# Performance work log

Hardware: AMD Instinct MI355X
Metric: run time of the kernel (lower is better)

The kernel has to match this reference:

```python
import jax, jax.numpy as jnp
import numpy as np

STRIDE = 4
IMG_H, IMG_W = 800, 1216
NMS_THRESH = 0.7
PRE_NMS = 1000
POST_NMS = 1000
MIN_SIZE = 0.0
SCALE_CLAMP = float(np.log(1000.0 / 16.0))  # detectron2 Box2BoxTransform clamp
A = 3  # anchors per location


def _cell_anchors():
    size = 32.0
    ars = jnp.array([0.5, 1.0, 2.0], jnp.float32)
    area = size * size
    w = jnp.sqrt(area / ars)
    h = ars * w
    return jnp.stack([-w / 2, -h / 2, w / 2, h / 2], axis=1)  # [A,4]


def _anchors(H, W):
    sx = jnp.arange(W, dtype=jnp.float32) * STRIDE
    sy = jnp.arange(H, dtype=jnp.float32) * STRIDE
    gy, gx = jnp.meshgrid(sy, sx, indexing='ij')
    shifts = jnp.stack([gx, gy, gx, gy], axis=-1).reshape(-1, 1, 4)  # [H*W,1,4]
    return (shifts + _cell_anchors()[None]).reshape(-1, 4)  # [H*W*A,4]


def _conv(x, w, b, pad):
    y = jax.lax.conv_general_dilated(x, w, (1, 1), pad,
                                     dimension_numbers=('NCHW', 'OIHW', 'NCHW'))
    return y + b[None, :, None, None]


def _decode(anchors, deltas):
    # anchors [M,4], deltas [N,M,4]; weights (1,1,1,1)
    wa = anchors[:, 2] - anchors[:, 0]
    ha = anchors[:, 3] - anchors[:, 1]
    cx = anchors[:, 0] + 0.5 * wa
    cy = anchors[:, 1] + 0.5 * ha
    dx, dy = deltas[..., 0], deltas[..., 1]
    dw = jnp.minimum(deltas[..., 2], SCALE_CLAMP)
    dh = jnp.minimum(deltas[..., 3], SCALE_CLAMP)
    px = dx * wa + cx
    py = dy * ha + cy
    pw = jnp.exp(dw) * wa
    ph = jnp.exp(dh) * ha
    return jnp.stack([px - 0.5 * pw, py - 0.5 * ph,
                      px + 0.5 * pw, py + 0.5 * ph], axis=-1)


def _iou_matrix(boxes):  # [K,4] -> [K,K]
    area = (boxes[:, 2] - boxes[:, 0]) * (boxes[:, 3] - boxes[:, 1])
    lt = jnp.maximum(boxes[:, None, :2], boxes[None, :, :2])
    rb = jnp.minimum(boxes[:, None, 2:], boxes[None, :, 2:])
    wh = jnp.clip(rb - lt, 0.0)
    inter = wh[..., 0] * wh[..., 1]
    return inter / jnp.maximum(area[:, None] + area[None, :] - inter, 1e-9)


def _nms_keep(boxes):
    # boxes already sorted by descending score; greedy NMS
    iou = _iou_matrix(boxes)
    K = boxes.shape[0]

    def step(sup, i):
        keep = ~sup[i]
        sup = sup | (keep & (iou[i] > NMS_THRESH))
        return sup, keep

    _, keep = jax.lax.scan(step, jnp.zeros(K, bool), jnp.arange(K))
    return keep


def setup_inputs() -> dict:
    key = jax.random.key(0)
    ks = jax.random.split(key, 4)
    features = jax.random.normal(ks[0], (2, 256, 200, 304), jnp.float32)
    w_conv = jax.random.normal(ks[1], (256, 256, 3, 3), jnp.float32) * 0.01
    b_conv = jnp.zeros((256,), jnp.float32)
    w_obj = jax.random.normal(ks[2], (3, 256, 1, 1), jnp.float32) * 0.01
    b_obj = jnp.zeros((3,), jnp.float32)
    w_delta = jax.random.normal(ks[3], (12, 256, 1, 1), jnp.float32) * 0.01
    b_delta = jnp.zeros((12,), jnp.float32)
    return {"features": features, "w_conv": w_conv, "b_conv": b_conv,
            "w_obj": w_obj, "b_obj": b_obj, "w_delta": w_delta, "b_delta": b_delta}


def reference(features, w_conv, b_conv, w_obj, b_obj, w_delta, b_delta):
    N, C, H, W = features.shape
    t = jax.nn.relu(_conv(features, w_conv, b_conv, 'SAME'))
    logits = _conv(t, w_obj, b_obj, 'VALID')            # [N,A,H,W]
    deltas = _conv(t, w_delta, b_delta, 'VALID')        # [N,4A,H,W]
    logits = logits.transpose(0, 2, 3, 1).reshape(N, -1)               # [N,H*W*A]
    deltas = deltas.reshape(N, A, 4, H, W).transpose(0, 3, 4, 1, 2).reshape(N, -1, 4)

    anchors = _anchors(H, W)                             # [H*W*A,4]
    boxes = _decode(anchors, deltas)                     # [N,M,4]
    boxes = jnp.stack([jnp.clip(boxes[..., 0], 0.0, IMG_W),
                       jnp.clip(boxes[..., 1], 0.0, IMG_H),
                       jnp.clip(boxes[..., 2], 0.0, IMG_W),
                       jnp.clip(boxes[..., 3], 0.0, IMG_H)], axis=-1)

    valid = ((boxes[..., 2] - boxes[..., 0]) >= MIN_SIZE) & \
            ((boxes[..., 3] - boxes[..., 1]) >= MIN_SIZE)
    scores = jnp.where(valid, logits, -jnp.inf)

    top_s, top_i = jax.lax.top_k(scores, PRE_NMS)                      # sorted desc
    top_b = jnp.take_along_axis(boxes, top_i[..., None], axis=1)       # [N,K,4]

    keep = jax.vmap(_nms_keep)(top_b)                                  # [N,K]
    s = jnp.where(keep, top_s, -jnp.inf)
    fin_s, fin_i = jax.lax.top_k(s, POST_NMS)                          # sorted desc (=final sort)
    fin_b = jnp.take_along_axis(top_b, fin_i[..., None], axis=1)
    fin_b = jnp.where(jnp.isfinite(fin_s)[..., None], fin_b, 0.0)
    return fin_b, fin_s
```

## Files before the change

kernel.cpp:

```cpp
#include <hip/hip_runtime.h>
#include <math.h>
#include <stdint.h>

#define CC 256
#define HH 200
#define WW 304
#define NN 2
#define HW 60800
#define MM 182400
#define KK 1000
#define HP 202
#define WP 306
#define SCALE_CLAMP_F 4.135166556742356f
#define NEG_SENTINEL -1.0e30f
#define CAND_CAP 2048

typedef __attribute__((ext_vector_type(8))) short short8;
typedef __attribute__((ext_vector_type(4))) float f32x4;

#define VMW(N) asm volatile("s_waitcnt vmcnt(" #N ")" ::: "memory")

__device__ __forceinline__ unsigned short f2bf(float f) {
  unsigned u = __float_as_uint(f);
  u += 0x7FFFu + ((u >> 16) & 1u);
  return (unsigned short)(u >> 16);
}
__device__ __forceinline__ unsigned int fkey(float s) {
  unsigned int u = __float_as_uint(s);
  return (u & 0x80000000u) ? ~u : (u | 0x80000000u);
}
__device__ __forceinline__ float iou_ref(float4 a, float4 b) {
#pragma clang fp contract(off)
  float areaA = (a.z - a.x) * (a.w - a.y);
  float areaB = (b.z - b.x) * (b.w - b.y);
  float ltx = fmaxf(a.x, b.x), lty = fmaxf(a.y, b.y);
  float rbx = fminf(a.z, b.z), rby = fminf(a.w, b.w);
  float w = fmaxf(rbx - ltx, 0.0f), h = fmaxf(rby - lty, 0.0f);
  float inter = w * h;
  float denom = fmaxf(areaA + areaB - inter, 1e-9f);
  return inter / denom;
}
__device__ __forceinline__ void gload16(const void* g, void* l) {
  __builtin_amdgcn_global_load_lds(
      (const __attribute__((address_space(1))) unsigned int*)g,
      (__attribute__((address_space(3))) unsigned int*)l, 16, 0, 0);
}
__device__ __forceinline__ int swz(int byte) {
  return byte ^ (((byte >> 7) & 7) << 4);
}

__global__ __launch_bounds__(256) void wt_pack(const float* __restrict__ w,
                                               unsigned short* __restrict__ wt_b) {
  int o = blockIdx.x * 256 + threadIdx.x;
  int cin = o & 255, cout = (o >> 8) & 255, pos = o >> 16;
  wt_b[o] = f2bf(w[(cout * 256 + cin) * 9 + pos]);
}

__global__ __launch_bounds__(256) void in_pack(const float* __restrict__ in,
                                               unsigned short* __restrict__ fbp) {
  __shared__ unsigned short tile[64][65];
  int tid = threadIdx.x;
  int p0 = blockIdx.x * 64;
  int c0 = blockIdx.y * 64;
  int n = blockIdx.z;
  int lane = tid & 63;
  int p = p0 + lane;
  int yp = 0, xp = 0;
  bool inb = false;
  if (p < HP * WP) {
    yp = p / WP; xp = p - yp * WP;
    inb = (yp >= 1 && yp <= HH && xp >= 1 && xp <= WW);
  }
  for (int ci = tid >> 6; ci < 64; ci += 4) {
    float v = 0.f;
    if (inb) v = in[(((size_t)n * CC + c0 + ci) * HH + (yp - 1)) * WW + (xp - 1)];
    tile[ci][lane] = f2bf(v);
  }
  __syncthreads();
  for (int i = 0; i < 4; ++i) {
    int idx4 = (i * 256 + tid) * 4;
    int hwi = idx4 >> 6, cb = idx4 & 63;
    int pp = p0 + hwi;
    if (pp < HP * WP) {
      ushort4 v;
      v.x = tile[cb][hwi]; v.y = tile[cb + 1][hwi];
      v.z = tile[cb + 2][hwi]; v.w = tile[cb + 3][hwi];
      *(ushort4*)&fbp[((size_t)n * HP * WP + pp) * 256 + c0 + cb] = v;
    }
  }
}

__global__ __launch_bounds__(256) void conv_mfma(
    const unsigned short* __restrict__ wt_b, const unsigned short* __restrict__ fbp,
    const float* __restrict__ bias, const float* __restrict__ w_obj,
    const float* __restrict__ w_delta, float* __restrict__ phead) {
  __shared__ __align__(16) unsigned short lA[3][4096];
  __shared__ __align__(16) unsigned short lB[2][5760];
  __shared__ float bl_l[128];
  int tid = threadIdx.x;
  int lane = tid & 63, wid = tid >> 6;
  int wm = wid >> 1, wn = wid & 1;
  int lrow = lane & 15, lgrp = lane >> 4;
  int zz = blockIdx.z;
  int n = zz >> 1, ct = zz & 1;
  int X0 = blockIdx.x * 16, Y0 = blockIdx.y * 8;

  f32x4 acc[4][4];
#pragma unroll
  for (int m = 0; m < 4; ++m)
#pragma unroll
    for (int r = 0; r < 4; ++r) acc[m][r] = {0.f, 0.f, 0.f, 0.f};

  if (tid < 128) bl_l[tid] = bias[ct * 128 + tid];

  auto stageA = [&](int pos, int cc, int buf) {
#pragma unroll
    for (int is = 0; is < 2; ++is) {
      int idx = is * 256 + tid;
      int L = swz(idx * 16);
      int cout = L >> 6, q = (L >> 4) & 3;
      const unsigned short* g =
          wt_b + (((size_t)pos * 256 + ct * 128 + cout) << 8) + cc * 32 + q * 8;
      gload16(g, (char*)&lA[buf][0] + is * 4096 + (wid << 10));
    }
  };
  auto stageB = [&](int cc, int buf) {
#pragma unroll
    for (int is = 0; is < 3; ++is) {
      int idx = is * 256 + tid;
      if (idx < 720) {
        int L = swz(idx * 16);
        int rc = L >> 6, q = (L >> 4) & 3;
        int row = rc / 18, col = rc - row * 18;
        const unsigned short* g =
            fbp + (((size_t)n * HP + Y0 + row) * WP + X0 + col) * 256 + cc * 32 + q * 8;
        gload16(g, (char*)&lB[buf][0] + is * 4096 + (wid << 10));
      }
    }
  };

  stageA(0, 0, 0);
  stageA(1, 0, 1);
  stageB(0, 0);
  __syncthreads();

#pragma unroll 1
  for (int cc = 0; cc < 8; ++cc) {
    const int bb = cc & 1;
    const bool ccl7 = (cc < 7);
#pragma unroll
    for (int pos = 0; pos < 9; ++pos) {
      {
        int pos2 = pos + 2, cc2 = cc;
        if (pos2 >= 9) { pos2 -= 9; cc2 += 1; }
        if (cc2 < 8) stageA(pos2, cc2, (pos + 2) % 3);
      }
      if (pos == 0 && ccl7) stageB(cc + 1, bb ^ 1);

      int ky = pos / 3, kx = pos - ky * 3;
      short8 af[4], bfr[4];
#pragma unroll
      for (int m = 0; m < 4; ++m) {
        int Lb = ((wm * 64 + m * 16 + lrow) << 6) + (lgrp << 4);
        af[m] = *(const short8*)((const char*)&lA[pos % 3][0] + swz(Lb));
      }
#pragma unroll
      for (int r = 0; r < 4; ++r) {
        int Lb = (((wn * 4 + r + ky) * 18 + lrow + kx) << 6) + (lgrp << 4);
        bfr[r] = *(const short8*)((const char*)&lB[bb][0] + swz(Lb));
      }
#pragma unroll
      for (int m = 0; m < 4; ++m)
#pragma unroll
        for (int r = 0; r < 4; ++r)
          acc[m][r] = __builtin_amdgcn_mfma_f32_16x16x32_bf16(af[m], bfr[r], acc[m][r], 0, 0, 0);

      if (pos < 2) {
        if (ccl7) VMW(5); else VMW(2);
      } else if (pos == 7) {
        if (ccl7) VMW(2); else VMW(0);
      } else {
        VMW(2);
      }
      __builtin_amdgcn_sched_barrier(0);
      __builtin_amdgcn_s_barrier();
      asm volatile("" ::: "memory");
    }
  }
  __syncthreads();

#pragma unroll
  for (int m = 0; m < 4; ++m)
#pragma unroll
    for (int j = 0; j < 4; ++j) {
      float b = bl_l[wm * 64 + m * 16 + (lgrp << 2) + j];
#pragma unroll
      for (int r = 0; r < 4; ++r) acc[m][r][j] = fmaxf(acc[m][r][j] + b, 0.f);
    }

  float* whl_l = (float*)&lA[0][0];
  for (int i = tid; i < 1920; i += 256) {
    int o = i >> 7, cl = i & 127;
    whl_l[i] = (o < 3) ? w_obj[o * 256 + ct * 128 + cl]
                       : w_delta[(o - 3) * 256 + ct * 128 + cl];
  }
  __syncthreads();

  float* hacc = (float*)&lB[0][0];
#pragma unroll 1
  for (int o = 0; o < 15; ++o) {
    float p0 = 0.f, p1 = 0.f, p2 = 0.f, p3 = 0.f;
#pragma unroll
    for (int m = 0; m < 4; ++m)
#pragma unroll
      for (int j = 0; j < 4; ++j) {
        float w = whl_l[o * 128 + wm * 64 + m * 16 + (lgrp << 2) + j];
        p0 = fmaf(w, acc[m][0][j], p0);
        p1 = fmaf(w, acc[m][1][j], p1);
        p2 = fmaf(w, acc[m][2][j], p2);
        p3 = fmaf(w, acc[m][3][j], p3);
      }
    p0 += __shfl_xor(p0, 16); p0 += __shfl_xor(p0, 32);
    p1 += __shfl_xor(p1, 16); p1 += __shfl_xor(p1, 32);
    p2 += __shfl_xor(p2, 16); p2 += __shfl_xor(p2, 32);
    p3 += __shfl_xor(p3, 16); p3 += __shfl_xor(p3, 32);
    if (lgrp == 0) {
      hacc[(((o * 8) + wn * 4 + 0) * 16 + lrow) * 2 + wm] = p0;
      hacc[(((o * 8) + wn * 4 + 1) * 16 + lrow) * 2 + wm] = p1;
      hacc[(((o * 8) + wn * 4 + 2) * 16 + lrow) * 2 + wm] = p2;
      hacc[(((o * 8) + wn * 4 + 3) * 16 + lrow) * 2 + wm] = p3;
    }
  }
  __syncthreads();

  if (tid < 128) {
    int row = tid >> 4, col = tid & 15;
    int loc = (Y0 + row) * WW + (X0 + col);
    size_t base = ((size_t)zz * 15) * HW + loc;
#pragma unroll
    for (int o = 0; o < 15; ++o) {
      const float* hp = &hacc[((o * 8 + row) * 16 + col) * 2];
      phead[base + (size_t)o * HW] = hp[0] + hp[1];
    }
  }
}

__global__ __launch_bounds__(256) void decode_kernel(
    const float* __restrict__ phead, const float* __restrict__ b_obj,
    const float* __restrict__ b_delta, float* __restrict__ scores,
    float* __restrict__ boxes, unsigned long long* __restrict__ keys,
    unsigned int* __restrict__ ghist) {
  __shared__ unsigned int hl[8192];
  int tid = threadIdx.x;
  for (int i = tid; i < 8192; i += 256) hl[i] = 0;
  __syncthreads();
  int n = blockIdx.y;
  int loc = blockIdx.x * 256 + tid;
  if (loc < HW) {
    float ho[15];
    const float* p0 = phead + ((size_t)(n * 2 + 0) * 15) * HW + loc;
    const float* p1 = phead + ((size_t)(n * 2 + 1) * 15) * HW + loc;
#pragma unroll
    for (int o = 0; o < 15; ++o) ho[o] = p0[(size_t)o * HW] + p1[(size_t)o * HW];
#pragma unroll
    for (int o = 0; o < 3; ++o) ho[o] += b_obj[o];
#pragma unroll
    for (int o = 0; o < 12; ++o) ho[3 + o] += b_delta[o];
    {
#pragma clang fp contract(off)
      int h = loc / WW, w = loc - h * WW;
      float gx = (float)(w * 4);
      float gy = (float)(h * 4);
      float s2048 = sqrtf(2048.0f), s512 = sqrtf(512.0f);
      float aw[3] = {s2048, 32.0f, s512};
      float ah[3] = {0.5f * s2048, 32.0f, 2.0f * s512};
#pragma unroll
      for (int a = 0; a < 3; ++a) {
        float ax1 = gx - 0.5f * aw[a], ay1 = gy - 0.5f * ah[a];
        float ax2 = gx + 0.5f * aw[a], ay2 = gy + 0.5f * ah[a];
        float wa = ax2 - ax1, ha = ay2 - ay1;
        float cx = ax1 + 0.5f * wa, cy = ay1 + 0.5f * ha;
        float dx = ho[3 + a * 4 + 0], dy = ho[3 + a * 4 + 1];
        float dw = fminf(ho[3 + a * 4 + 2], SCALE_CLAMP_F);
        float dh = fminf(ho[3 + a * 4 + 3], SCALE_CLAMP_F);
        float px = dx * wa + cx, py = dy * ha + cy;
        float pw = expf(dw) * wa, ph = expf(dh) * ha;
        float x1 = px - 0.5f * pw, y1 = py - 0.5f * ph;
        float x2v = px + 0.5f * pw, y2v = py + 0.5f * ph;
        x1 = fminf(fmaxf(x1, 0.f), 1216.f);
        y1 = fminf(fmaxf(y1, 0.f), 800.f);
        x2v = fminf(fmaxf(x2v, 0.f), 1216.f);
        y2v = fminf(fmaxf(y2v, 0.f), 800.f);
        int m = loc * 3 + a;
        ((float4*)boxes)[(size_t)n * MM + m] = make_float4(x1, y1, x2v, y2v);
        float sc = ho[a];
        scores[(size_t)n * MM + m] = sc;
        unsigned long long k =
            ((unsigned long long)fkey(sc) << 18) | (unsigned long long)(262143 - m);
        keys[(size_t)n * MM + m] = k;
        atomicAdd(&hl[(unsigned)(k >> 37)], 1u);
      }
    }
  }
  __syncthreads();
  for (int i = tid; i < 8192; i += 256) {
    unsigned v = hl[i];
    if (v) atomicAdd(&ghist[n * 8192 + i], v);
  }
}

__global__ __launch_bounds__(256) void gather_kernel(
    const unsigned long long* __restrict__ keys, const unsigned int* __restrict__ ghist,
    unsigned int* __restrict__ cnt, unsigned long long* __restrict__ cand) {
  __shared__ unsigned int ps[256];
  __shared__ int bsh;
  int n = blockIdx.y, tid = threadIdx.x;
  const unsigned int* h = ghist + n * 8192;
  unsigned s = 0;
  for (int k = 0; k < 32; ++k) s += h[tid * 32 + k];
  ps[tid] = s;
  __syncthreads();
  if (tid == 0) {
    unsigned cum = 0; int b = 0;
    for (int t = 255; t >= 0; --t) {
      if (cum + ps[t] >= KK) {
        for (int bin = t * 32 + 31; bin >= t * 32; --bin) {
          cum += h[bin];
          if (cum >= KK) { b = bin; break; }
        }
        break;
      }
      cum += ps[t];
    }
    bsh = b;
  }
  __syncthreads();
  int b = bsh;
  const unsigned long long* kp = keys + (size_t)n * MM;
  int i0 = blockIdx.x * 2850, i1 = min(i0 + 2850, MM);
  for (int i = i0 + tid; i < i1; i += 256) {
    unsigned long long k = kp[i];
    if ((int)(unsigned)(k >> 37) >= b) {
      unsigned pos = atomicAdd(&cnt[n], 1u);
      if (pos < CAND_CAP) cand[(size_t)n * CAND_CAP + pos] = k;
    }
  }
}

__global__ __launch_bounds__(1024) void final_select(
    const unsigned long long* __restrict__ cand, const unsigned int* __restrict__ cnt,
    const float* __restrict__ scores, const float* __restrict__ boxes,
    float* __restrict__ s_scores, float* __restrict__ s_boxes) {
  __shared__ unsigned long long sel[CAND_CAP];
  int n = blockIdx.x, tid = threadIdx.x;
  int E = (int)min(cnt[n], (unsigned)CAND_CAP);
  for (int i = tid; i < CAND_CAP; i += 1024)
    sel[i] = (i < E) ? cand[(size_t)n * CAND_CAP + i] : 0ull;
  __syncthreads();
  for (unsigned k2 = 2; k2 <= CAND_CAP; k2 <<= 1) {
    for (unsigned j = k2 >> 1; j > 0; j >>= 1) {
      for (int i = tid; i < CAND_CAP; i += 1024) {
        int l = i ^ (int)j;
        if (l > i) {
          unsigned long long a = sel[i], bb = sel[l];
          bool sw = ((i & k2) == 0) ? (a < bb) : (a > bb);
          if (sw) { sel[i] = bb; sel[l] = a; }
        }
      }
      __syncthreads();
    }
  }
  if (tid < KK) {
    unsigned long long k = sel[tid];
    int m = 262143 - (int)(k & 0x3FFFFull);
    s_scores[n * KK + tid] = scores[(size_t)n * MM + m];
    ((float4*)s_boxes)[n * KK + tid] = ((const float4*)boxes)[(size_t)n * MM + m];
  }
}

__global__ __launch_bounds__(256) void mask_kernel(const float* __restrict__ s_boxes,
                                                   unsigned long long* __restrict__ mask) {
  int i = blockIdx.x, n = blockIdx.y;
  int tid = threadIdx.x, w = tid >> 6, lane = tid & 63;
  const float4* bp = (const float4*)s_boxes + n * KK;
  float4 bi = bp[i];
#pragma unroll
  for (int p = 0; p < 4; ++p) {
    int word = p * 4 + w;
    int j = word * 64 + lane;
    bool over = false;
    if (j < KK) {
      float4 bj = bp[j];
      over = iou_ref(bi, bj) > 0.7f;
    }
    unsigned long long bal = __ballot(over);
    if (lane == 0) mask[((size_t)n * KK + i) * 16 + word] = bal;
  }
}

__global__ __launch_bounds__(1024) void scan_write_kernel(
    const float* __restrict__ s_scores, const float* __restrict__ s_boxes,
    const unsigned long long* __restrict__ mask, float* __restrict__ out) {
  int n = blockIdx.x, tid = threadIdx.x;
  int wid = tid >> 6, lane = tid & 63;
  __shared__ unsigned long long swl[16];
  __shared__ unsigned long long keepw[16];
  __shared__ unsigned int wpre[17];
  if (tid < 16) swl[tid] = 0ull;
  __syncthreads();
  const unsigned long long* mrow = mask + (size_t)n * 16000;
  for (int c = 0; c < 16; ++c) {
    int i = c * 64 + lane;
    unsigned long long myword = (i < KK) ? mrow[(size_t)i * 16 + wid] : 0ull;
    if (wid == 0) {
      unsigned long long m = (i < KK) ? mrow[(size_t)i * 16 + c] : 0ull;
      unsigned long long cur = swl[c];
      unsigned long long kw = 0ull;
      int lim = min(64, KK - c * 64);
      for (int b = 0; b < lim; ++b) {
        unsigned long long mb = __shfl(m, b);
        if (!((cur >> b) & 1ull)) { kw |= (1ull << b); cur |= mb; }
      }
      if (lane == 0) keepw[c] = kw;
    }
    __syncthreads();
    unsigned long long kw = keepw[c];
    unsigned long long v = ((kw >> lane) & 1ull) ? myword : 0ull;
#pragma unroll
    for (int s = 32; s > 0; s >>= 1) v |= __shfl_xor(v, s);
    if (lane == 0) swl[wid] |= v;
    __syncthreads();
  }
  if (tid == 0) {
    unsigned int c = 0;
    for (int w2 = 0; w2 < 16; ++w2) { wpre[w2] = c; c += (unsigned int)__popcll(keepw[w2]); }
    wpre[16] = c;
  }
  __syncthreads();
  if (tid < KK) {
    int word = tid >> 6, bit = tid & 63;
    unsigned long long kwv = keepw[word];
    bool kept = (kwv >> bit) & 1ull;
    unsigned int before = wpre[word] + (unsigned int)__popcll(kwv & ((1ull << bit) - 1ull));
    unsigned int nk = wpre[16];
    unsigned int dst = kept ? before : nk + ((unsigned int)tid - before);
    float4 b = kept ? ((const float4*)s_boxes)[n * KK + tid] : make_float4(0.f, 0.f, 0.f, 0.f);
    float s = kept ? s_scores[n * KK + tid] : NEG_SENTINEL;
    ((float4*)out)[n * KK + dst] = b;
    out[8000 + n * KK + dst] = s;
  }
}

extern "C" void kernel_launch(void* const* d_in, const int* in_sizes, int n_in,
                              void* d_out, int out_size, void* d_ws, size_t ws_size,
                              hipStream_t stream) {
  (void)in_sizes; (void)n_in; (void)out_size; (void)ws_size;
  const float* features = (const float*)d_in[0];
  const float* w_conv   = (const float*)d_in[1];
  const float* b_conv   = (const float*)d_in[2];
  const float* w_obj    = (const float*)d_in[3];
  const float* b_obj    = (const float*)d_in[4];
  const float* w_delta  = (const float*)d_in[5];
  const float* b_delta  = (const float*)d_in[6];

  char* ws = (char*)d_ws;
  unsigned short* wt_b = (unsigned short*)ws;
  unsigned short* fbp  = (unsigned short*)(ws + 1179648);
  char* O = ws + 64475136;
  float* phead = (float*)O;
  float* scores = (float*)(O + 14592000);
  float* boxes  = (float*)(O + 16051200);
  unsigned long long* keys = (unsigned long long*)(O + 21888000);
  char* P = O + 24806400;
  unsigned int* ghist = (unsigned int*)P;
  unsigned int* cnt = (unsigned int*)(P + 65536);
  unsigned long long* cand = (unsigned long long*)(P + 65792);
  float* s_scores = (float*)(P + 98560);
  float* s_boxes  = (float*)(P + 106752);
  unsigned long long* maskbuf = (unsigned long long*)(P + 139264);
  float* out = (float*)d_out;

  wt_pack<<<2304, 256, 0, stream>>>(w_conv, wt_b);
  in_pack<<<dim3(966, 4, 2), 256, 0, stream>>>(features, fbp);
  hipMemsetAsync(ghist, 0, 65536 + 256, stream);
  conv_mfma<<<dim3(19, 25, 4), 256, 0, stream>>>(wt_b, fbp, b_conv, w_obj, w_delta, phead);
  decode_kernel<<<dim3(238, 2), 256, 0, stream>>>(phead, b_obj, b_delta,
                                                  scores, boxes, keys, ghist);
  gather_kernel<<<dim3(64, 2), 256, 0, stream>>>(keys, ghist, cnt, cand);
  final_select<<<2, 1024, 0, stream>>>(cand, cnt, scores, boxes, s_scores, s_boxes);
  mask_kernel<<<dim3(1000, 2), 256, 0, stream>>>(s_boxes, maskbuf);
  scan_write_kernel<<<2, 1024, 0, stream>>>(s_scores, s_boxes, maskbuf, out);
}
```

Measured before the change: 395.6 us.

## Merge pack kernels, simplify conv pipeline, and fuse NMS mask into scan

Three changes land together. The weight pack, input pack and histogram memset become one launch. The conv inner loop drops from a three-stage A buffer with hand-tuned vmcnt waits to two-stage double buffering with plain __syncthreads. The separate IoU mask kernel is removed, and the NMS scan computes IoUs on the fly from boxes held in LDS. This cuts launch overhead and the global mask round trip, but the conv loop loses some latency hiding and the NMS now runs on only two blocks.

```diff
diff --git a/kernel.cpp b/kernel.cpp
--- a/kernel.cpp
+++ b/kernel.cpp
@@ -18,8 +18,6 @@
 typedef __attribute__((ext_vector_type(8))) short short8;
 typedef __attribute__((ext_vector_type(4))) float f32x4;
 
-#define VMW(N) asm volatile("s_waitcnt vmcnt(" #N ")" ::: "memory")
-
 __device__ __forceinline__ unsigned short f2bf(float f) {
   unsigned u = __float_as_uint(f);
   u += 0x7FFFu + ((u >> 16) & 1u);
@@ -49,44 +47,51 @@
   return byte ^ (((byte >> 7) & 7) << 4);
 }
 
-__global__ __launch_bounds__(256) void wt_pack(const float* __restrict__ w,
-                                               unsigned short* __restrict__ wt_b) {
-  int o = blockIdx.x * 256 + threadIdx.x;
-  int cin = o & 255, cout = (o >> 8) & 255, pos = o >> 16;
-  wt_b[o] = f2bf(w[(cout * 256 + cin) * 9 + pos]);
-}
-
-__global__ __launch_bounds__(256) void in_pack(const float* __restrict__ in,
-                                               unsigned short* __restrict__ fbp) {
+__global__ __launch_bounds__(256) void pack_kernel(
+    const float* __restrict__ w, unsigned short* __restrict__ wt_b,
+    const float* __restrict__ in, unsigned short* __restrict__ fbp,
+    unsigned int* __restrict__ ghist, unsigned int* __restrict__ cnt) {
   __shared__ unsigned short tile[64][65];
+  int b = blockIdx.x;
   int tid = threadIdx.x;
-  int p0 = blockIdx.x * 64;
-  int c0 = blockIdx.y * 64;
-  int n = blockIdx.z;
-  int lane = tid & 63;
-  int p = p0 + lane;
-  int yp = 0, xp = 0;
-  bool inb = false;
-  if (p < HP * WP) {
-    yp = p / WP; xp = p - yp * WP;
-    inb = (yp >= 1 && yp <= HH && xp >= 1 && xp <= WW);
-  }
-  for (int ci = tid >> 6; ci < 64; ci += 4) {
-    float v = 0.f;
-    if (inb) v = in[(((size_t)n * CC + c0 + ci) * HH + (yp - 1)) * WW + (xp - 1)];
-    tile[ci][lane] = f2bf(v);
-  }
-  __syncthreads();
-  for (int i = 0; i < 4; ++i) {
-    int idx4 = (i * 256 + tid) * 4;
-    int hwi = idx4 >> 6, cb = idx4 & 63;
-    int pp = p0 + hwi;
-    if (pp < HP * WP) {
-      ushort4 v;
-      v.x = tile[cb][hwi]; v.y = tile[cb + 1][hwi];
-      v.z = tile[cb + 2][hwi]; v.w = tile[cb + 3][hwi];
-      *(ushort4*)&fbp[((size_t)n * HP * WP + pp) * 256 + c0 + cb] = v;
-    }
+  if (b < 2304) {
+    int o = b * 256 + tid;
+    int cin = o & 255, cout = (o >> 8) & 255, pos = o >> 16;
+    wt_b[o] = f2bf(w[(cout * 256 + cin) * 9 + pos]);
+  } else if (b < 10032) {
+    int bb = b - 2304;
+    int bx = bb % 966, rem = bb / 966;
+    int by = rem & 3, n = rem >> 2;
+    int p0 = bx * 64, c0 = by * 64;
+    int lane = tid & 63;
+    int p = p0 + lane;
+    int yp = 0, xp = 0;
+    bool inb = false;
+    if (p < HP * WP) {
+      yp = p / WP; xp = p - yp * WP;
+      inb = (yp >= 1 && yp <= HH && xp >= 1 && xp <= WW);
+    }
+    for (int ci = tid >> 6; ci < 64; ci += 4) {
+      float v = 0.f;
+      if (inb) v = in[(((size_t)n * CC + c0 + ci) * HH + (yp - 1)) * WW + (xp - 1)];
+      tile[ci][lane] = f2bf(v);
+    }
+    __syncthreads();
+    for (int i = 0; i < 4; ++i) {
+      int idx4 = (i * 256 + tid) * 4;
+      int hwi = idx4 >> 6, cb = idx4 & 63;
+      int pp = p0 + hwi;
+      if (pp < HP * WP) {
+        ushort4 v;
+        v.x = tile[cb][hwi]; v.y = tile[cb + 1][hwi];
+        v.z = tile[cb + 2][hwi]; v.w = tile[cb + 3][hwi];
+        *(ushort4*)&fbp[((size_t)n * HP * WP + pp) * 256 + c0 + cb] = v;
+      }
+    }
+  } else {
+    int i = (b - 10032) * 256 + tid;
+    ghist[i] = 0;
+    if (i < 2) cnt[i] = 0;
   }
 }
 
@@ -94,7 +99,7 @@
     const unsigned short* __restrict__ wt_b, const unsigned short* __restrict__ fbp,
     const float* __restrict__ bias, const float* __restrict__ w_obj,
     const float* __restrict__ w_delta, float* __restrict__ phead) {
-  __shared__ __align__(16) unsigned short lA[3][4096];
+  __shared__ __align__(16) unsigned short lA[2][4096];
   __shared__ __align__(16) unsigned short lB[2][5760];
   __shared__ float bl_l[128];
   int tid = threadIdx.x;
@@ -140,29 +145,24 @@
   };
 
   stageA(0, 0, 0);
-  stageA(1, 0, 1);
   stageB(0, 0);
   __syncthreads();
 
+  int ab = 0;
 #pragma unroll 1
   for (int cc = 0; cc < 8; ++cc) {
-    const int bb = cc & 1;
-    const bool ccl7 = (cc < 7);
+    int bb = cc & 1;
 #pragma unroll
     for (int pos = 0; pos < 9; ++pos) {
-      {
-        int pos2 = pos + 2, cc2 = cc;
-        if (pos2 >= 9) { pos2 -= 9; cc2 += 1; }
-        if (cc2 < 8) stageA(pos2, cc2, (pos + 2) % 3);
-      }
-      if (pos == 0 && ccl7) stageB(cc + 1, bb ^ 1);
-
+      if (pos < 8) stageA(pos + 1, cc, ab ^ 1);
+      else if (cc < 7) stageA(0, cc + 1, ab ^ 1);
+      if (pos == 0 && cc < 7) stageB(cc + 1, bb ^ 1);
       int ky = pos / 3, kx = pos - ky * 3;
       short8 af[4], bfr[4];
 #pragma unroll
       for (int m = 0; m < 4; ++m) {
         int Lb = ((wm * 64 + m * 16 + lrow) << 6) + (lgrp << 4);
-        af[m] = *(const short8*)((const char*)&lA[pos % 3][0] + swz(Lb));
+        af[m] = *(const short8*)((const char*)&lA[ab][0] + swz(Lb));
       }
 #pragma unroll
       for (int r = 0; r < 4; ++r) {
@@ -174,20 +174,10 @@
 #pragma unroll
         for (int r = 0; r < 4; ++r)
           acc[m][r] = __builtin_amdgcn_mfma_f32_16x16x32_bf16(af[m], bfr[r], acc[m][r], 0, 0, 0);
-
-      if (pos < 2) {
-        if (ccl7) VMW(5); else VMW(2);
-      } else if (pos == 7) {
-        if (ccl7) VMW(2); else VMW(0);
-      } else {
-        VMW(2);
-      }
-      __builtin_amdgcn_sched_barrier(0);
-      __builtin_amdgcn_s_barrier();
-      asm volatile("" ::: "memory");
-    }
-  }
-  __syncthreads();
+      __syncthreads();
+      ab ^= 1;
+    }
+  }
 
 #pragma unroll
   for (int m = 0; m < 4; ++m)
@@ -378,57 +368,49 @@
   }
 }
 
-__global__ __launch_bounds__(256) void mask_kernel(const float* __restrict__ s_boxes,
-                                                   unsigned long long* __restrict__ mask) {
-  int i = blockIdx.x, n = blockIdx.y;
-  int tid = threadIdx.x, w = tid >> 6, lane = tid & 63;
-  const float4* bp = (const float4*)s_boxes + n * KK;
-  float4 bi = bp[i];
-#pragma unroll
-  for (int p = 0; p < 4; ++p) {
-    int word = p * 4 + w;
-    int j = word * 64 + lane;
-    bool over = false;
-    if (j < KK) {
-      float4 bj = bp[j];
-      over = iou_ref(bi, bj) > 0.7f;
-    }
-    unsigned long long bal = __ballot(over);
-    if (lane == 0) mask[((size_t)n * KK + i) * 16 + word] = bal;
-  }
-}
-
-__global__ __launch_bounds__(1024) void scan_write_kernel(
+__global__ __launch_bounds__(1024) void nms_kernel(
     const float* __restrict__ s_scores, const float* __restrict__ s_boxes,
-    const unsigned long long* __restrict__ mask, float* __restrict__ out) {
+    float* __restrict__ out) {
   int n = blockIdx.x, tid = threadIdx.x;
   int wid = tid >> 6, lane = tid & 63;
+  __shared__ float4 bx[KK];
   __shared__ unsigned long long swl[16];
   __shared__ unsigned long long keepw[16];
   __shared__ unsigned int wpre[17];
+  for (int i = tid; i < KK; i += 1024) bx[i] = ((const float4*)s_boxes)[n * KK + i];
   if (tid < 16) swl[tid] = 0ull;
   __syncthreads();
-  const unsigned long long* mrow = mask + (size_t)n * 16000;
   for (int c = 0; c < 16; ++c) {
-    int i = c * 64 + lane;
-    unsigned long long myword = (i < KK) ? mrow[(size_t)i * 16 + wid] : 0ull;
+    int lim = min(64, KK - c * 64);
     if (wid == 0) {
-      unsigned long long m = (i < KK) ? mrow[(size_t)i * 16 + c] : 0ull;
-      unsigned long long cur = swl[c];
-      unsigned long long kw = 0ull;
-      int lim = min(64, KK - c * 64);
-      for (int b = 0; b < lim; ++b) {
-        unsigned long long mb = __shfl(m, b);
-        if (!((cur >> b) & 1ull)) { kw |= (1ull << b); cur |= mb; }
+      int r = c * 64 + lane;
+      bool rv = r < KK;
+      float4 bi = rv ? bx[r] : make_float4(0.f, 0.f, 0.f, 0.f);
+      unsigned long long wrd = 0ull;
+      for (int j = 0; j < lim; ++j)
+        if (rv && iou_ref(bi, bx[c * 64 + j]) > 0.7f) wrd |= (1ull << j);
+      unsigned long long cur = swl[c], kw = 0ull;
+      for (int bbit = 0; bbit < lim; ++bbit) {
+        unsigned long long mb = __shfl(wrd, bbit);
+        if (!((cur >> bbit) & 1ull)) { kw |= (1ull << bbit); cur |= mb; }
       }
       if (lane == 0) keepw[c] = kw;
     }
     __syncthreads();
     unsigned long long kw = keepw[c];
-    unsigned long long v = ((kw >> lane) & 1ull) ? myword : 0ull;
-#pragma unroll
-    for (int s = 32; s > 0; s >>= 1) v |= __shfl_xor(v, s);
-    if (lane == 0) swl[wid] |= v;
+    int j = wid * 64 + lane;
+    bool jv = j < KK;
+    float4 bj = jv ? bx[j] : make_float4(0.f, 0.f, 0.f, 0.f);
+    bool sup = false;
+    unsigned long long t = kw;
+    while (t) {
+      int bbit = __ffsll((unsigned long long)t) - 1;
+      t &= t - 1;
+      float4 br = bx[c * 64 + bbit];
+      if (iou_ref(br, bj) > 0.7f) sup = true;
+    }
+    unsigned long long bal = __ballot(sup && jv);
+    if (lane == 0) swl[wid] |= bal;
     __syncthreads();
   }
   if (tid == 0) {
@@ -444,7 +426,7 @@
     unsigned int before = wpre[word] + (unsigned int)__popcll(kwv & ((1ull << bit) - 1ull));
     unsigned int nk = wpre[16];
     unsigned int dst = kept ? before : nk + ((unsigned int)tid - before);
-    float4 b = kept ? ((const float4*)s_boxes)[n * KK + tid] : make_float4(0.f, 0.f, 0.f, 0.f);
+    float4 b = kept ? bx[tid] : make_float4(0.f, 0.f, 0.f, 0.f);
     float s = kept ? s_scores[n * KK + tid] : NEG_SENTINEL;
     ((float4*)out)[n * KK + dst] = b;
     out[8000 + n * KK + dst] = s;
@@ -477,17 +459,13 @@
   unsigned long long* cand = (unsigned long long*)(P + 65792);
   float* s_scores = (float*)(P + 98560);
   float* s_boxes  = (float*)(P + 106752);
-  unsigned long long* maskbuf = (unsigned long long*)(P + 139264);
   float* out = (float*)d_out;
 
-  wt_pack<<<2304, 256, 0, stream>>>(w_conv, wt_b);
-  in_pack<<<dim3(966, 4, 2), 256, 0, stream>>>(features, fbp);
-  hipMemsetAsync(ghist, 0, 65536 + 256, stream);
+  pack_kernel<<<10096, 256, 0, stream>>>(w_conv, wt_b, features, fbp, ghist, cnt);
   conv_mfma<<<dim3(19, 25, 4), 256, 0, stream>>>(wt_b, fbp, b_conv, w_obj, w_delta, phead);
   decode_kernel<<<dim3(238, 2), 256, 0, stream>>>(phead, b_obj, b_delta,
                                                   scores, boxes, keys, ghist);
   gather_kernel<<<dim3(64, 2), 256, 0, stream>>>(keys, ghist, cnt, cand);
   final_select<<<2, 1024, 0, stream>>>(cand, cnt, scores, boxes, s_scores, s_boxes);
-  mask_kernel<<<dim3(1000, 2), 256, 0, stream>>>(s_boxes, maskbuf);
-  scan_write_kernel<<<2, 1024, 0, stream>>>(s_scores, s_boxes, maskbuf, out);
-}
+  nms_kernel<<<2, 1024, 0, stream>>>(s_scores, s_boxes, out);
+}
```

Result: slower. 693.0 us (+75.2%).
